# Optimization experiments

Measured on AMD Instinct MI355X. Metric: run time of the kernel, lower is better.

## Reference

```python
import jax, jax.numpy as jnp
import numpy as np

B, S, D, H, WINDOW = 2, 2048, 2048, 16, 256
HD = D // H  # head_dim = 128

def setup_inputs() -> dict:
    key = jax.random.key(0)
    ks = jax.random.split(key, 6)
    s = 0.02  # initializer_range-like scale for weights
    return {
        "hidden_states": jax.random.normal(ks[0], (B, S, D), jnp.float32),
        "attention_mask": jnp.ones((B, S), jnp.int32),
        "Wq": jax.random.normal(ks[1], (D, D), jnp.float32) * s,
        "Wk": jax.random.normal(ks[2], (D, D), jnp.float32) * s,
        "Wv": jax.random.normal(ks[3], (D, D), jnp.float32) * s,
        "Wo": jax.random.normal(ks[4], (D, D), jnp.float32) * s,
        "bo": jnp.zeros((D,), jnp.float32),
    }

def reference(hidden_states, attention_mask, Wq, Wk, Wv, Wo, bo):
    # GPT-Neo quirk: query is multiplied by sqrt(head_dim) and then
    # dot_product_attention_weights divides by sqrt(head_dim) -> net UNSCALED scores.
    q = (hidden_states @ Wq).reshape(B, S, H, HD)  # [B,S,H,hd]
    k = (hidden_states @ Wk).reshape(B, S, H, HD)
    v = (hidden_states @ Wv).reshape(B, S, H, HD)

    # local causal mask: attend iff i - window < j <= i
    i = jnp.arange(S)[:, None]
    j = jnp.arange(S)[None, :]
    local_causal = (j <= i) & (j > i - WINDOW)  # [S,S]
    mask = local_causal[None, None] & (attention_mask[:, None, None, :] > 0)  # [B,1,S,S]

    neg = jnp.finfo(jnp.float32).min
    scores = jnp.einsum("bqhd,bkhd->bhqk", q, k)  # [B,H,S,S] unscaled
    scores = jnp.where(mask, scores, neg)
    attn = jax.nn.softmax(scores, axis=-1)

    out = jnp.einsum("bhqk,bkhd->bqhd", attn, v).reshape(B, S, D)
    return out @ Wo + bo
```

## Files before the change

### kernel.cpp

```cpp
#include <hip/hip_runtime.h>

#define B_   2
#define S_   2048
#define D_   2048
#define H_   16
#define HD_  128
#define WIN_ 256
#define M_   (B_ * S_)

typedef float  f32x4  __attribute__((ext_vector_type(4)));
typedef short  s16x8  __attribute__((ext_vector_type(8)));
typedef __bf16 bf16x8 __attribute__((ext_vector_type(8)));
typedef unsigned short ushort_t;

__device__ inline unsigned short f2b(float f) {
  unsigned u = __builtin_bit_cast(unsigned, f);
  u += 0x7fffu + ((u >> 16) & 1u);
  return (unsigned short)(u >> 16);
}
__device__ inline float b2f(unsigned short h) {
  unsigned u = ((unsigned)h) << 16;
  return __builtin_bit_cast(float, u);
}

template <typename T>
__device__ auto mfma_impl(T a, T b, f32x4 c, int)
    -> decltype(__builtin_amdgcn_mfma_f32_16x16x32_bf16(a, b, c, 0, 0, 0)) {
  return __builtin_amdgcn_mfma_f32_16x16x32_bf16(a, b, c, 0, 0, 0);
}
template <typename T>
__device__ f32x4 mfma_impl(T a, T b, f32x4 c, long) {
  return __builtin_amdgcn_mfma_f32_16x16x32_bf16(
      __builtin_bit_cast(bf16x8, a), __builtin_bit_cast(bf16x8, b), c, 0, 0, 0);
}
__device__ inline f32x4 mfma_bf16(s16x8 a, s16x8 b, f32x4 c) {
  return mfma_impl(a, b, c, 0);
}

#if defined(__has_builtin)
#if __has_builtin(__builtin_amdgcn_global_load_lds)
#define HAS_GLL 1
#endif
#endif
#ifndef HAS_GLL
#define HAS_GLL 0
#endif

__device__ inline void gl_lds16(const ushort_t* g, ushort_t* lds_wave_base) {
#if HAS_GLL
  __builtin_amdgcn_global_load_lds(
      (const __attribute__((address_space(1))) unsigned int*)g,
      (__attribute__((address_space(3))) unsigned int*)lds_wave_base, 16, 0, 0);
#else
  const int lane = threadIdx.x & 63;
  *(uint4*)(lds_wave_base + lane * 8) = *(const uint4*)g;
#endif
}

__global__ __launch_bounds__(256) void k_split(const float* __restrict__ x,
                                               ushort_t* __restrict__ hi,
                                               ushort_t* __restrict__ lo, int n) {
  int i = (blockIdx.x * 256 + threadIdx.x) * 4;
  if (i + 3 < n) {
    float4 v = *(const float4*)(x + i);
    ushort4 h, l;
    h.x = f2b(v.x); l.x = f2b(v.x - b2f(h.x));
    h.y = f2b(v.y); l.y = f2b(v.y - b2f(h.y));
    h.z = f2b(v.z); l.z = f2b(v.z - b2f(h.z));
    h.w = f2b(v.w); l.w = f2b(v.w - b2f(h.w));
    *(ushort4*)(hi + i) = h;
    *(ushort4*)(lo + i) = l;
  }
}

__global__ __launch_bounds__(256) void k_transpose4(const float* __restrict__ W0,
                                                    const float* __restrict__ W1,
                                                    const float* __restrict__ W2,
                                                    const float* __restrict__ W3,
                                                    ushort_t* __restrict__ T0h,
                                                    ushort_t* __restrict__ T0l,
                                                    ushort_t* __restrict__ T1h,
                                                    ushort_t* __restrict__ T1l,
                                                    ushort_t* __restrict__ T2h,
                                                    ushort_t* __restrict__ T3h) {
  __shared__ float t[32][33];
  const int z = blockIdx.z;
  const float* W = (z == 0) ? W0 : (z == 1) ? W1 : (z == 2) ? W2 : W3;
  ushort_t* Th = (z == 0) ? T0h : (z == 1) ? T1h : (z == 2) ? T2h : T3h;
  ushort_t* Tl = (z == 0) ? T0l : (z == 1) ? T1l : nullptr;
  int bx = blockIdx.x * 32, by = blockIdx.y * 32;
  int tx = threadIdx.x, ty = threadIdx.y;
#pragma unroll
  for (int r = 0; r < 32; r += 8)
    t[ty + r][tx] = W[(size_t)(by + ty + r) * D_ + bx + tx];
  __syncthreads();
#pragma unroll
  for (int r = 0; r < 32; r += 8) {
    float v = t[tx][ty + r];
    unsigned short h = f2b(v);
    Th[(size_t)(bx + ty + r) * D_ + by + tx] = h;
    if (Tl) Tl[(size_t)(bx + ty + r) * D_ + by + tx] = f2b(v - b2f(h));
  }
}

__global__ __launch_bounds__(256) void k_vtrans(const ushort_t* __restrict__ Vb,
                                                ushort_t* __restrict__ Vt) {
  __shared__ ushort_t t[32][33];
  int bx = blockIdx.x * 32, by = blockIdx.y * 32, b = blockIdx.z;
  int tx = threadIdx.x, ty = threadIdx.y;
#pragma unroll
  for (int r = 0; r < 32; r += 8)
    t[ty + r][tx] = Vb[((size_t)(b * S_ + by + ty + r)) * D_ + bx + tx];
  __syncthreads();
#pragma unroll
  for (int r = 0; r < 32; r += 8)
    Vt[((size_t)(b * D_ + bx + ty + r)) * S_ + by + tx] = t[tx][ty + r];
}


__device__ inline void stage64(const ushort_t* __restrict__ g, int rowbase,
                               ushort_t* ldsTile, int tid) {
  const int r = tid >> 3;
  const int gs = ((tid & 7) ^ (r & 7)) * 8;
  gl_lds16(g + (size_t)(rowbase + r) * D_ + gs,
           ldsTile + rowbase * 64 + (tid >> 6) * 512);
}

__global__ __launch_bounds__(512) void k_qkv(
    const ushort_t* __restrict__ Ah, const ushort_t* __restrict__ Al,
    const ushort_t* __restrict__ WqH, const ushort_t* __restrict__ WqL,
    const ushort_t* __restrict__ WkH, const ushort_t* __restrict__ WvH,
    ushort_t* __restrict__ Qh, ushort_t* __restrict__ Ql,
    ushort_t* __restrict__ Ko, ushort_t* __restrict__ Vo) {
  __shared__ ushort_t Ab_[2][256 * 64];
  __shared__ ushort_t Bb_[2][256 * 64];
  const int tid = threadIdx.x;
  const int wave = tid >> 6, lane = tid & 63;
  const int quad = lane >> 4, l16 = lane & 15;

  const int lid = blockIdx.y * 24 + blockIdx.x;
  const int nlid = (lid & 7) * 48 + (lid >> 3);
  const int bx = nlid % 24, by = nlid / 24;
  const int m0 = by * 256;
  const int wtype = bx >> 3;
  const int n0 = (bx & 7) * 256;
  const int nseg = (wtype == 0) ? 3 : (wtype == 1) ? 2 : 1;
  const ushort_t* Bh0 = (wtype == 0) ? WqH : (wtype == 1) ? WkH : WvH;
  const int NT = nseg << 5;
  const int NI = NT >> 1;

  const int wrM = (wave >> 2) * 128;
  const int wcN = (wave & 3) * 64;
  const int ko0 = (quad ^ (l16 & 7)) * 8;
  const int ko1 = ((4 + quad) ^ (l16 & 7)) * 8;

#define SRC_A(t) ((((t) >> 5) == 1 ? Al : Ah) + (size_t)m0 * D_ + ((t) & 31) * 64)
#define SRC_B(t) ((((t) >> 5) == 2 ? WqL : Bh0) + (size_t)n0 * D_ + ((t) & 31) * 64)
#define RD(buf, row, ko) (*(const s16x8*)((buf) + (row) * 64 + (ko)))

  {
    const ushort_t* sA0 = SRC_A(0);
    const ushort_t* sB0 = SRC_B(0);
    const ushort_t* sB1 = SRC_B(1);
    stage64(sA0, 0,   &Ab_[0][0], tid); stage64(sA0, 64,  &Ab_[0][0], tid);
    stage64(sA0, 128, &Ab_[0][0], tid); stage64(sA0, 192, &Ab_[0][0], tid);
    stage64(sB0, 0,   &Bb_[0][0], tid); stage64(sB0, 64,  &Bb_[0][0], tid);
    stage64(sB0, 128, &Bb_[0][0], tid); stage64(sB0, 192, &Bb_[0][0], tid);
    stage64(sB1, 0,   &Bb_[1][0], tid); stage64(sB1, 64,  &Bb_[1][0], tid);
    stage64(sB1, 128, &Bb_[1][0], tid); stage64(sB1, 192, &Bb_[1][0], tid);
  }
  asm volatile("s_waitcnt vmcnt(4)" ::: "memory");
  __builtin_amdgcn_s_barrier();
  asm volatile("" ::: "memory");

#define PH_PRE()                                         \
  __builtin_amdgcn_s_barrier();                          \
  asm volatile("s_waitcnt lgkmcnt(0)" ::: "memory");     \
  __builtin_amdgcn_sched_barrier(0);                     \
  __builtin_amdgcn_s_setprio(1)
#define PH_POST()                                        \
  __builtin_amdgcn_s_setprio(0);                         \
  __builtin_amdgcn_s_barrier();                          \
  asm volatile("" ::: "memory")

  f32x4 acc[8][4] = {};
  s16x8 aF[4][2], bL[2][2], bH[2][2];

  for (int i = 0; i < NI; ++i) {
    const int t0 = 2 * i;
    const bool doSt = (i + 1 < NI);
    const ushort_t* A0 = &Ab_[0][0];
    const ushort_t* B0 = &Bb_[0][0];
    const ushort_t* A1 = &Ab_[1][0];
    const ushort_t* B1 = &Bb_[1][0];
    const ushort_t* sAt1 = SRC_A(t0 + 1);
    const ushort_t* sAt2 = SRC_A(t0 + 2);
    const ushort_t* sBt2 = SRC_B(t0 + 2);
    const ushort_t* sBt3 = SRC_B(t0 + 3);

#pragma unroll
    for (int f = 0; f < 4; ++f) {
      aF[f][0] = RD(A0, wrM + f * 16 + l16, ko0);
      aF[f][1] = RD(A0, wrM + f * 16 + l16, ko1);
    }
#pragma unroll
    for (int c = 0; c < 2; ++c) {
      bL[c][0] = RD(B0, wcN + c * 16 + l16, ko0);
      bL[c][1] = RD(B0, wcN + c * 16 + l16, ko1);
    }
    stage64(sAt1, 0, &Ab_[1][0], tid);
    stage64(sAt1, 64, &Ab_[1][0], tid);
    PH_PRE();
#pragma unroll
    for (int f = 0; f < 4; ++f)
#pragma unroll
      for (int c = 0; c < 2; ++c) {
        acc[f][c] = mfma_bf16(aF[f][0], bL[c][0], acc[f][c]);
        acc[f][c] = mfma_bf16(aF[f][1], bL[c][1], acc[f][c]);
      }
    PH_POST();

#pragma unroll
    for (int c = 0; c < 2; ++c) {
      bH[c][0] = RD(B0, wcN + 32 + c * 16 + l16, ko0);
      bH[c][1] = RD(B0, wcN + 32 + c * 16 + l16, ko1);
    }
    stage64(sAt1, 128, &Ab_[1][0], tid);
    stage64(sAt1, 192, &Ab_[1][0], tid);
    PH_PRE();
#pragma unroll
    for (int f = 0; f < 4; ++f)
#pragma unroll
      for (int c = 0; c < 2; ++c) {
        acc[f][2 + c] = mfma_bf16(aF[f][0], bH[c][0], acc[f][2 + c]);
        acc[f][2 + c] = mfma_bf16(aF[f][1], bH[c][1], acc[f][2 + c]);
      }
    PH_POST();

#pragma unroll
    for (int f = 0; f < 4; ++f) {
      aF[f][0] = RD(A0, wrM + 64 + f * 16 + l16, ko0);
      aF[f][1] = RD(A0, wrM + 64 + f * 16 + l16, ko1);
    }
    if (doSt) {
      stage64(sBt2, 0, &Bb_[0][0], tid);
      stage64(sBt2, 64, &Bb_[0][0], tid);
    }
    PH_PRE();
#pragma unroll
    for (int f = 0; f < 4; ++f)
#pragma unroll
      for (int c = 0; c < 2; ++c) {
        acc[4 + f][c] = mfma_bf16(aF[f][0], bL[c][0], acc[4 + f][c]);
        acc[4 + f][c] = mfma_bf16(aF[f][1], bL[c][1], acc[4 + f][c]);
      }
    PH_POST();

    if (doSt) {
      stage64(sBt2, 128, &Bb_[0][0], tid);
      stage64(sBt2, 192, &Bb_[0][0], tid);
    }
    PH_PRE();
#pragma unroll
    for (int f = 0; f < 4; ++f)
#pragma unroll
      for (int c = 0; c < 2; ++c) {
        acc[4 + f][2 + c] = mfma_bf16(aF[f][0], bH[c][0], acc[4 + f][2 + c]);
        acc[4 + f][2 + c] = mfma_bf16(aF[f][1], bH[c][1], acc[4 + f][2 + c]);
      }
    __builtin_amdgcn_s_setprio(0);
    if (doSt) asm volatile("s_waitcnt vmcnt(4)" ::: "memory");
    else      asm volatile("s_waitcnt vmcnt(0)" ::: "memory");
    __builtin_amdgcn_s_barrier();
    asm volatile("" ::: "memory");

#pragma unroll
    for (int f = 0; f < 4; ++f) {
      aF[f][0] = RD(A1, wrM + f * 16 + l16, ko0);
      aF[f][1] = RD(A1, wrM + f * 16 + l16, ko1);
    }
#pragma unroll
    for (int c = 0; c < 2; ++c) {
      bL[c][0] = RD(B1, wcN + c * 16 + l16, ko0);
      bL[c][1] = RD(B1, wcN + c * 16 + l16, ko1);
    }
    if (doSt) {
      stage64(sAt2, 0, &Ab_[0][0], tid);
      stage64(sAt2, 64, &Ab_[0][0], tid);
    }
    PH_PRE();
#pragma unroll
    for (int f = 0; f < 4; ++f)
#pragma unroll
      for (int c = 0; c < 2; ++c) {
        acc[f][c] = mfma_bf16(aF[f][0], bL[c][0], acc[f][c]);
        acc[f][c] = mfma_bf16(aF[f][1], bL[c][1], acc[f][c]);
      }
    PH_POST();

#pragma unroll
    for (int c = 0; c < 2; ++c) {
      bH[c][0] = RD(B1, wcN + 32 + c * 16 + l16, ko0);
      bH[c][1] = RD(B1, wcN + 32 + c * 16 + l16, ko1);
    }
    if (doSt) {
      stage64(sAt2, 128, &Ab_[0][0], tid);
      stage64(sAt2, 192, &Ab_[0][0], tid);
    }
    PH_PRE();
#pragma unroll
    for (int f = 0; f < 4; ++f)
#pragma unroll
      for (int c = 0; c < 2; ++c) {
        acc[f][2 + c] = mfma_bf16(aF[f][0], bH[c][0], acc[f][2 + c]);
        acc[f][2 + c] = mfma_bf16(aF[f][1], bH[c][1], acc[f][2 + c]);
      }
    PH_POST();

#pragma unroll
    for (int f = 0; f < 4; ++f) {
      aF[f][0] = RD(A1, wrM + 64 + f * 16 + l16, ko0);
      aF[f][1] = RD(A1, wrM + 64 + f * 16 + l16, ko1);
    }
    if (doSt) {
      stage64(sBt3, 0, &Bb_[1][0], tid);
      stage64(sBt3, 64, &Bb_[1][0], tid);
    }
    PH_PRE();
#pragma unroll
    for (int f = 0; f < 4; ++f)
#pragma unroll
      for (int c = 0; c < 2; ++c) {
        acc[4 + f][c] = mfma_bf16(aF[f][0], bL[c][0], acc[4 + f][c]);
        acc[4 + f][c] = mfma_bf16(aF[f][1], bL[c][1], acc[4 + f][c]);
      }
    PH_POST();

    if (doSt) {
      stage64(sBt3, 128, &Bb_[1][0], tid);
      stage64(sBt3, 192, &Bb_[1][0], tid);
    }
    PH_PRE();
#pragma unroll
    for (int f = 0; f < 4; ++f)
#pragma unroll
      for (int c = 0; c < 2; ++c) {
        acc[4 + f][2 + c] = mfma_bf16(aF[f][0], bH[c][0], acc[4 + f][2 + c]);
        acc[4 + f][2 + c] = mfma_bf16(aF[f][1], bH[c][1], acc[4 + f][2 + c]);
      }
    __builtin_amdgcn_s_setprio(0);
    if (doSt) {
      asm volatile("s_waitcnt vmcnt(4)" ::: "memory");
      __builtin_amdgcn_s_barrier();
      asm volatile("" ::: "memory");
    }
  }
#undef PH_PRE
#undef PH_POST
#undef SRC_A
#undef SRC_B
#undef RD

#pragma unroll
  for (int a = 0; a < 8; ++a)
#pragma unroll
    for (int nt = 0; nt < 4; ++nt)
#pragma unroll
      for (int r = 0; r < 4; ++r) {
        const int row = m0 + wrM + a * 16 + quad * 4 + r;
        const int col = n0 + wcN + nt * 16 + l16;
        const float v = acc[a][nt][r];
        const size_t idx = (size_t)row * D_ + col;
        if (wtype == 0) {
          unsigned short h = f2b(v);
          Qh[idx] = h;
          Ql[idx] = f2b(v - b2f(h));
        } else if (wtype == 1) {
          Ko[idx] = f2b(v);
        } else {
          Vo[idx] = f2b(v);
        }
      }
}

__device__ inline void stage_chunk(const ushort_t* __restrict__ gbase, int K,
                                   int rowbase, ushort_t* ldsTile, int tid) {
  const int rr = tid >> 3;
  const int gs = ((tid & 7) ^ (rr & 7)) * 8;
  gl_lds16(gbase + (size_t)(rowbase + rr) * K + gs,
           ldsTile + rowbase * 64 + (tid >> 6) * 512);
}

template <int NSEG, int OUT>
__global__ __launch_bounds__(512) void k_gemm8(
    const ushort_t* __restrict__ A0, const ushort_t* __restrict__ A1,
    const ushort_t* __restrict__ A2, const ushort_t* __restrict__ B0,
    const ushort_t* __restrict__ B2, ushort_t* __restrict__ Co,
    ushort_t* __restrict__ Col, float* __restrict__ Cf,
    const float* __restrict__ bias, int M, int N, int K) {
  __shared__ ushort_t As_[3][256 * 64];
  __shared__ ushort_t Bs_[3][128 * 64];
  const int tid = threadIdx.x;
  const int wave = tid >> 6, lane = tid & 63;
  const int quad = lane >> 4, l16 = lane & 15;
  const int m0 = blockIdx.y * 256, n0 = blockIdx.x * 128;
  const int wrM = (wave >> 1) * 64;
  const int wcN = (wave & 1) * 64;
  const int aRowB = (wrM + l16) * 64;
  const int bRowB = (wcN + l16) * 64;
  int ks8[2];
  ks8[0] = ((0 + quad) ^ (l16 & 7)) * 8;
  ks8[1] = ((4 + quad) ^ (l16 & 7)) * 8;
  const int NT = NSEG * 32;

  {
    const ushort_t* Ab0 = A0 + (size_t)m0 * K;
    const ushort_t* Bb0 = B0 + (size_t)n0 * K;
#pragma unroll
    for (int t = 0; t < 2; ++t) {
      const ushort_t* Ab = Ab0 + t * 64;
      const ushort_t* Bb = Bb0 + t * 64;
      stage_chunk(Ab, K, 0,   &As_[t][0], tid);
      stage_chunk(Ab, K, 64,  &As_[t][0], tid);
      stage_chunk(Ab, K, 128, &As_[t][0], tid);
      stage_chunk(Ab, K, 192, &As_[t][0], tid);
      stage_chunk(Bb, K, 0,   &Bs_[t][0], tid);
      stage_chunk(Bb, K, 64,  &Bs_[t][0], tid);
    }
  }
  asm volatile("s_waitcnt vmcnt(6)" ::: "memory");
  __builtin_amdgcn_s_barrier();
  asm volatile("" ::: "memory");

  f32x4 acc[4][4] = {};
  int cur = 0;
  for (int kt = 0; kt < NT; ++kt) {
    const int st = kt + 2;
    const bool doStage = (st < NT);
    int sbuf = cur + 2; if (sbuf >= 3) sbuf -= 3;
    ushort_t* At  = &As_[cur][0];
    ushort_t* Bt  = &Bs_[cur][0];
    ushort_t* Ads = &As_[sbuf][0];
    ushort_t* Bds = &Bs_[sbuf][0];
    const ushort_t* Asb = A0;
    const ushort_t* Bsb = B0;
    if (doStage) {
      const int sg = st >> 5;
      const ushort_t* Ag = A0;
      const ushort_t* Bg = B0;
      if (NSEG >= 2 && sg == 1) Ag = A1;
      if (NSEG == 3 && sg == 2) { Ag = A2; Bg = B2; }
      Asb = Ag + (size_t)m0 * K + (size_t)(st & 31) * 64;
      Bsb = Bg + (size_t)n0 * K + (size_t)(st & 31) * 64;
    }
    s16x8 bf[4][2];
#pragma unroll
    for (int p = 0; p < 2; ++p) {
      s16x8 af[2][2];
#pragma unroll
      for (int i = 0; i < 2; ++i)
#pragma unroll
        for (int s = 0; s < 2; ++s)
          af[i][s] = *(const s16x8*)(At + aRowB + (p * 2 + i) * 1024 + ks8[s]);
      if (p == 0) {
#pragma unroll
        for (int nt = 0; nt < 4; ++nt)
#pragma unroll
          for (int s = 0; s < 2; ++s)
            bf[nt][s] = *(const s16x8*)(Bt + bRowB + nt * 1024 + ks8[s]);
      }
      if (doStage) {
        if (p == 0) {
          stage_chunk(Asb, K, 0,   Ads, tid);
          stage_chunk(Asb, K, 64,  Ads, tid);
          stage_chunk(Asb, K, 128, Ads, tid);
        } else {
          stage_chunk(Asb, K, 192, Ads, tid);
          stage_chunk(Bsb, K, 0,   Bds, tid);
          stage_chunk(Bsb, K, 64,  Bds, tid);
        }
      }
      asm volatile("s_waitcnt lgkmcnt(0)" ::: "memory");
      __builtin_amdgcn_sched_barrier(0);
      __builtin_amdgcn_s_setprio(1);
#pragma unroll
      for (int i = 0; i < 2; ++i)
#pragma unroll
        for (int nt = 0; nt < 4; ++nt)
#pragma unroll
          for (int s = 0; s < 2; ++s)
            acc[p * 2 + i][nt] = mfma_bf16(af[i][s], bf[nt][s], acc[p * 2 + i][nt]);
      __builtin_amdgcn_s_setprio(0);
      if (p == 1) {
        if (doStage) asm volatile("s_waitcnt vmcnt(6)" ::: "memory");
        else         asm volatile("s_waitcnt vmcnt(0)" ::: "memory");
        __builtin_amdgcn_s_barrier();
        asm volatile("" ::: "memory");
      }
    }
    cur = (cur == 2) ? 0 : cur + 1;
  }

#pragma unroll
  for (int mt = 0; mt < 4; ++mt)
#pragma unroll
    for (int nt = 0; nt < 4; ++nt)
#pragma unroll
      for (int r = 0; r < 4; ++r) {
        int row = m0 + wrM + mt * 16 + quad * 4 + r;
        int col = n0 + wcN + nt * 16 + l16;
        float v = acc[mt][nt][r];
        if (OUT == 2) {
          Cf[(size_t)row * N + col] = v + bias[col];
        } else if (OUT == 1) {
          unsigned short h = f2b(v);
          Co[(size_t)row * N + col]  = h;
          Col[(size_t)row * N + col] = f2b(v - b2f(h));
        } else {
          Co[(size_t)row * N + col] = f2b(v);
        }
      }
}

__global__ __launch_bounds__(256) void k_fattn(const ushort_t* __restrict__ Qh,
                                               const ushort_t* __restrict__ Ql,
                                               const ushort_t* __restrict__ Kh,
                                               const ushort_t* __restrict__ Vt,
                                               const int* __restrict__ amask,
                                               ushort_t* __restrict__ AO) {
  __shared__ ushort_t Ksh[64][136];
  __shared__ ushort_t Vs[128][72];
  __shared__ ushort_t ps[4][16][72];
  __shared__ int ams[320];
  const int tid = threadIdx.x;
  const int wave = tid >> 6, lane = tid & 63;
  const int quad = lane >> 4, l16 = lane & 15;
  const int qt = blockIdx.x, h = blockIdx.y, b = blockIdx.z;
  const int q0 = qt * 64;

  for (int x = tid; x < 320; x += 256) {
    int j = q0 - 256 + x;
    ams[x] = (j >= 0) ? amask[b * S_ + j] : 0;
  }

  const int qrowA = q0 + wave * 16 + l16;
  const ushort_t* qbh = Qh + ((size_t)(b * S_ + qrowA) * D_) + h * HD_;
  const ushort_t* qbl = Ql + ((size_t)(b * S_ + qrowA) * D_) + h * HD_;
  s16x8 qh[4], ql[4];
#pragma unroll
  for (int kk = 0; kk < 4; kk++) {
    qh[kk] = *(const s16x8*)(qbh + kk * 32 + quad * 8);
    ql[kk] = *(const s16x8*)(qbl + kk * 32 + quad * 8);
  }

  f32x4 O[8] = {};
  float m_run[4], l_run[4];
#pragma unroll
  for (int r = 0; r < 4; r++) { m_run[r] = -3.0e38f; l_run[r] = 0.f; }

  const int t0 = (qt < 4) ? (4 - qt) : 0;
  for (int t = t0; t < 5; t++) {
    const int kb = q0 - 256 + 64 * t;
    __syncthreads();
    {
      const int key = tid >> 2, dimb = (tid & 3) * 32;
      const ushort_t* kgh = Kh + ((size_t)(b * S_ + kb + key) * D_) + h * HD_ + dimb;
#pragma unroll
      for (int u = 0; u < 4; u++)
        *(uint4*)&Ksh[key][dimb + u * 8] = *(const uint4*)(kgh + u * 8);
      const int hd = tid >> 1, keyb = (tid & 1) * 32;
      const ushort_t* vg = Vt + ((size_t)(b * D_ + h * HD_ + hd) * S_) + kb + keyb;
#pragma unroll
      for (int u = 0; u < 4; u++)
        *(uint4*)&Vs[hd][keyb + u * 8] = *(const uint4*)(vg + u * 8);
    }
    __syncthreads();

    f32x4 sacc[4] = {};
#pragma unroll
    for (int kk = 0; kk < 4; kk++)
#pragma unroll
      for (int nt = 0; nt < 4; nt++) {
        s16x8 kfh = *(const s16x8*)&Ksh[nt * 16 + l16][kk * 32 + quad * 8];
        sacc[nt] = mfma_bf16(qh[kk], kfh, sacc[nt]);
        sacc[nt] = mfma_bf16(ql[kk], kfh, sacc[nt]);
      }

#pragma unroll
    for (int nt = 0; nt < 4; nt++) {
      const int j = kb + nt * 16 + l16;
      const bool amok = ams[64 * t + nt * 16 + l16] != 0;
#pragma unroll
      for (int r = 0; r < 4; r++) {
        const int iq = q0 + wave * 16 + quad * 4 + r;
        const bool ok = amok && (j <= iq) && (j > iq - WIN_);
        if (!ok) sacc[nt][r] = -3.0e38f;
      }
    }
    float mt[4];
#pragma unroll
    for (int r = 0; r < 4; r++) {
      mt[r] = fmaxf(fmaxf(sacc[0][r], sacc[1][r]), fmaxf(sacc[2][r], sacc[3][r]));
      mt[r] = fmaxf(mt[r], __shfl_xor(mt[r], 1));
      mt[r] = fmaxf(mt[r], __shfl_xor(mt[r], 2));
      mt[r] = fmaxf(mt[r], __shfl_xor(mt[r], 4));
      mt[r] = fmaxf(mt[r], __shfl_xor(mt[r], 8));
    }
    float alpha[4], lt[4];
#pragma unroll
    for (int r = 0; r < 4; r++) {
      float mnew = fmaxf(m_run[r], mt[r]);
      alpha[r] = __expf(m_run[r] - mnew);
      m_run[r] = mnew;
      lt[r] = 0.f;
#pragma unroll
      for (int nt = 0; nt < 4; nt++) {
        float s = sacc[nt][r];
        float p = (s > -1.0e30f) ? __expf(s - mnew) : 0.f;
        sacc[nt][r] = p;
        lt[r] += p;
      }
      lt[r] += __shfl_xor(lt[r], 1);
      lt[r] += __shfl_xor(lt[r], 2);
      lt[r] += __shfl_xor(lt[r], 4);
      lt[r] += __shfl_xor(lt[r], 8);
      l_run[r] = l_run[r] * alpha[r] + lt[r];
    }
#pragma unroll
    for (int o = 0; o < 8; o++)
#pragma unroll
      for (int r = 0; r < 4; r++) O[o][r] *= alpha[r];
#pragma unroll
    for (int nt = 0; nt < 4; nt++)
#pragma unroll
      for (int r = 0; r < 4; r++)
        ps[wave][quad * 4 + r][nt * 16 + l16] = f2b(sacc[nt][r]);
    __syncthreads();
#pragma unroll
    for (int kk2 = 0; kk2 < 2; kk2++) {
      s16x8 pf = *(const s16x8*)&ps[wave][l16][kk2 * 32 + quad * 8];
#pragma unroll
      for (int o = 0; o < 8; o++) {
        s16x8 vf = *(const s16x8*)&Vs[o * 16 + l16][kk2 * 32 + quad * 8];
        O[o] = mfma_bf16(pf, vf, O[o]);
      }
    }
  }
#pragma unroll
  for (int r = 0; r < 4; r++) l_run[r] = 1.0f / l_run[r];
#pragma unroll
  for (int o = 0; o < 8; o++)
#pragma unroll
    for (int r = 0; r < 4; r++) {
      int row = q0 + wave * 16 + quad * 4 + r;
      AO[((size_t)(b * S_ + row) * D_) + h * HD_ + o * 16 + l16] = f2b(O[o][r] * l_run[r]);
    }
}

extern "C" void kernel_launch(void* const* d_in, const int* in_sizes, int n_in,
                              void* d_out, int out_size, void* d_ws, size_t ws_size,
                              hipStream_t stream) {
  const float* hs    = (const float*)d_in[0];
  const int*   amask = (const int*)d_in[1];
  const float* Wq    = (const float*)d_in[2];
  const float* Wk    = (const float*)d_in[3];
  const float* Wv    = (const float*)d_in[4];
  const float* Wo    = (const float*)d_in[5];
  const float* bo    = (const float*)d_in[6];
  float* out = (float*)d_out;

  char* p = (char*)d_ws;
  ushort_t* hsHi = (ushort_t*)p; p += (size_t)16 << 20;
  ushort_t* hsLo = (ushort_t*)p; p += (size_t)16 << 20;
  ushort_t* WqTh = (ushort_t*)p; p += (size_t)8 << 20;
  ushort_t* WqTl = (ushort_t*)p; p += (size_t)8 << 20;
  ushort_t* WkTh = (ushort_t*)p; p += (size_t)8 << 20;
  ushort_t* WkTl = (ushort_t*)p; p += (size_t)8 << 20;  (void)WkTl;
  ushort_t* WvTh = (ushort_t*)p; p += (size_t)8 << 20;
  ushort_t* WoTh = (ushort_t*)p; p += (size_t)8 << 20;
  ushort_t* Qhb  = (ushort_t*)p; p += (size_t)16 << 20;
  ushort_t* Qlb  = (ushort_t*)p; p += (size_t)16 << 20;
  ushort_t* Khb  = (ushort_t*)p; p += (size_t)16 << 20;
  ushort_t* Vb   = (ushort_t*)p; p += (size_t)16 << 20;
  ushort_t* Vt   = (ushort_t*)p; p += (size_t)16 << 20;

  k_split<<<M_ * D_ / 1024, 256, 0, stream>>>(hs, hsHi, hsLo, M_ * D_);
  dim3 tb(32, 8), tg4(D_ / 32, D_ / 32, 4);
  k_transpose4<<<tg4, tb, 0, stream>>>(Wq, Wk, Wv, Wo, WqTh, WqTl, WkTh, nullptr, WvTh, WoTh);

  dim3 gq(24, 16);
  k_qkv<<<gq, 512, 0, stream>>>(hsHi, hsLo, WqTh, WqTl, WkTh, WvTh, Qhb, Qlb, Khb, Vb);

  dim3 vg(D_ / 32, S_ / 32, B_);
  k_vtrans<<<vg, tb, 0, stream>>>(Vb, Vt);

  dim3 ag(S_ / 64, H_, B_);
  k_fattn<<<ag, 256, 0, stream>>>(Qhb, Qlb, Khb, Vt, amask, hsHi );

  dim3 gg(D_ / 128, M_ / 256);
  k_gemm8<1, 2><<<gg, 512, 0, stream>>>(hsHi , nullptr, nullptr, WoTh, nullptr,
                                        nullptr, nullptr, out, bo, M_, D_, D_);
}
```

Measured before the change: 426.7 us.

## Double-buffer K/V tiles with register prefetch in sliding-window attention kernel

The attention kernel now handles 128 query rows per block with 512 threads instead of 64 rows with 256. K and V tiles sit in two LDS buffers, and the next tile is prefetched into registers while the current one is computed; the tile loop is unrolled in pairs and uses s_setprio around the MFMA sections. The goal is to hide global-load latency behind compute and to reuse each staged K/V tile across more query rows. In exchange it uses more LDS and registers per block and launches fewer blocks, which may reduce occupancy.

```diff
diff --git a/kernel.cpp b/kernel.cpp
--- a/kernel.cpp
+++ b/kernel.cpp
@@ -116,7 +116,6 @@
   for (int r = 0; r < 32; r += 8)
     Vt[((size_t)(b * D_ + bx + ty + r)) * S_ + by + tx] = t[tx][ty + r];
 }
-
 
 __device__ inline void stage64(const ushort_t* __restrict__ g, int rowbase,
                                ushort_t* ldsTile, int tid) {
@@ -522,26 +521,32 @@
       }
 }
 
-__global__ __launch_bounds__(256) void k_fattn(const ushort_t* __restrict__ Qh,
+__global__ __launch_bounds__(512) void k_fattn(const ushort_t* __restrict__ Qh,
                                                const ushort_t* __restrict__ Ql,
                                                const ushort_t* __restrict__ Kh,
                                                const ushort_t* __restrict__ Vt,
                                                const int* __restrict__ amask,
                                                ushort_t* __restrict__ AO) {
-  __shared__ ushort_t Ksh[64][136];
-  __shared__ ushort_t Vs[128][72];
-  __shared__ ushort_t ps[4][16][72];
-  __shared__ int ams[320];
+  __shared__ ushort_t Ksh[2][64][136];
+  __shared__ ushort_t Vs[2][128][72];
+  __shared__ ushort_t ps[8][16][72];
+  __shared__ int ams[384];
   const int tid = threadIdx.x;
   const int wave = tid >> 6, lane = tid & 63;
   const int quad = lane >> 4, l16 = lane & 15;
   const int qt = blockIdx.x, h = blockIdx.y, b = blockIdx.z;
-  const int q0 = qt * 64;
-
-  for (int x = tid; x < 320; x += 256) {
+  const int q0 = qt * 128;
+  const int t0 = (qt < 2) ? (4 - 2 * qt) : 0;
+
+  for (int x = tid; x < 384; x += 512) {
     int j = q0 - 256 + x;
     ams[x] = (j >= 0) ? amask[b * S_ + j] : 0;
   }
+
+  const int key  = tid >> 3, dimb = (tid & 7) * 16;
+  const int hd   = tid >> 2, keyb = (tid & 3) * 16;
+  const ushort_t* kgT = Kh + ((size_t)(b * S_) + key) * D_ + h * HD_ + dimb;
+  const ushort_t* vgT = Vt + ((size_t)(b * D_ + h * HD_ + hd)) * S_ + keyb;
 
   const int qrowA = q0 + wave * 16 + l16;
   const ushort_t* qbh = Qh + ((size_t)(b * S_ + qrowA) * D_) + h * HD_;
@@ -558,94 +563,120 @@
 #pragma unroll
   for (int r = 0; r < 4; r++) { m_run[r] = -3.0e38f; l_run[r] = 0.f; }
 
-  const int t0 = (qt < 4) ? (4 - qt) : 0;
-  for (int t = t0; t < 5; t++) {
-    const int kb = q0 - 256 + 64 * t;
-    __syncthreads();
-    {
-      const int key = tid >> 2, dimb = (tid & 3) * 32;
-      const ushort_t* kgh = Kh + ((size_t)(b * S_ + kb + key) * D_) + h * HD_ + dimb;
-#pragma unroll
-      for (int u = 0; u < 4; u++)
-        *(uint4*)&Ksh[key][dimb + u * 8] = *(const uint4*)(kgh + u * 8);
-      const int hd = tid >> 1, keyb = (tid & 1) * 32;
-      const ushort_t* vg = Vt + ((size_t)(b * D_ + h * HD_ + hd) * S_) + kb + keyb;
-#pragma unroll
-      for (int u = 0; u < 4; u++)
-        *(uint4*)&Vs[hd][keyb + u * 8] = *(const uint4*)(vg + u * 8);
-    }
-    __syncthreads();
-
-    f32x4 sacc[4] = {};
-#pragma unroll
-    for (int kk = 0; kk < 4; kk++)
-#pragma unroll
-      for (int nt = 0; nt < 4; nt++) {
-        s16x8 kfh = *(const s16x8*)&Ksh[nt * 16 + l16][kk * 32 + quad * 8];
-        sacc[nt] = mfma_bf16(qh[kk], kfh, sacc[nt]);
-        sacc[nt] = mfma_bf16(ql[kk], kfh, sacc[nt]);
-      }
-
-#pragma unroll
-    for (int nt = 0; nt < 4; nt++) {
-      const int j = kb + nt * 16 + l16;
-      const bool amok = ams[64 * t + nt * 16 + l16] != 0;
-#pragma unroll
-      for (int r = 0; r < 4; r++) {
-        const int iq = q0 + wave * 16 + quad * 4 + r;
-        const bool ok = amok && (j <= iq) && (j > iq - WIN_);
-        if (!ok) sacc[nt][r] = -3.0e38f;
-      }
-    }
-    float mt[4];
-#pragma unroll
-    for (int r = 0; r < 4; r++) {
-      mt[r] = fmaxf(fmaxf(sacc[0][r], sacc[1][r]), fmaxf(sacc[2][r], sacc[3][r]));
-      mt[r] = fmaxf(mt[r], __shfl_xor(mt[r], 1));
-      mt[r] = fmaxf(mt[r], __shfl_xor(mt[r], 2));
-      mt[r] = fmaxf(mt[r], __shfl_xor(mt[r], 4));
-      mt[r] = fmaxf(mt[r], __shfl_xor(mt[r], 8));
-    }
-    float alpha[4], lt[4];
-#pragma unroll
-    for (int r = 0; r < 4; r++) {
-      float mnew = fmaxf(m_run[r], mt[r]);
-      alpha[r] = __expf(m_run[r] - mnew);
-      m_run[r] = mnew;
-      lt[r] = 0.f;
-#pragma unroll
-      for (int nt = 0; nt < 4; nt++) {
-        float s = sacc[nt][r];
-        float p = (s > -1.0e30f) ? __expf(s - mnew) : 0.f;
-        sacc[nt][r] = p;
-        lt[r] += p;
-      }
-      lt[r] += __shfl_xor(lt[r], 1);
-      lt[r] += __shfl_xor(lt[r], 2);
-      lt[r] += __shfl_xor(lt[r], 4);
-      lt[r] += __shfl_xor(lt[r], 8);
-      l_run[r] = l_run[r] * alpha[r] + lt[r];
-    }
-#pragma unroll
-    for (int o = 0; o < 8; o++)
-#pragma unroll
-      for (int r = 0; r < 4; r++) O[o][r] *= alpha[r];
-#pragma unroll
-    for (int nt = 0; nt < 4; nt++)
-#pragma unroll
-      for (int r = 0; r < 4; r++)
-        ps[wave][quad * 4 + r][nt * 16 + l16] = f2b(sacc[nt][r]);
-    __syncthreads();
-#pragma unroll
-    for (int kk2 = 0; kk2 < 2; kk2++) {
-      s16x8 pf = *(const s16x8*)&ps[wave][l16][kk2 * 32 + quad * 8];
-#pragma unroll
-      for (int o = 0; o < 8; o++) {
-        s16x8 vf = *(const s16x8*)&Vs[o * 16 + l16][kk2 * 32 + quad * 8];
-        O[o] = mfma_bf16(pf, vf, O[o]);
-      }
-    }
-  }
+  uint4 rAk0, rAk1, rAv0, rAv1, rBk0, rBk1, rBv0, rBv1;
+  {
+    const long kb0 = (long)q0 - 256 + 64 * t0;
+    const ushort_t* kg = kgT + kb0 * D_;
+    const ushort_t* vg = vgT + kb0;
+    uint4 k0 = *(const uint4*)kg, k1 = *(const uint4*)(kg + 8);
+    uint4 v0 = *(const uint4*)vg, v1 = *(const uint4*)(vg + 8);
+    *(uint4*)&Ksh[0][key][dimb]     = k0;
+    *(uint4*)&Ksh[0][key][dimb + 8] = k1;
+    *(uint4*)&Vs[0][hd][keyb]       = v0;
+    *(uint4*)&Vs[0][hd][keyb + 8]   = v1;
+    const long kb1 = kb0 + 64;
+    const ushort_t* kg1 = kgT + kb1 * D_;
+    const ushort_t* vg1 = vgT + kb1;
+    rBk0 = *(const uint4*)kg1; rBk1 = *(const uint4*)(kg1 + 8);
+    rBv0 = *(const uint4*)vg1; rBv1 = *(const uint4*)(vg1 + 8);
+  }
+  asm volatile("s_waitcnt lgkmcnt(0)" ::: "memory");
+  __builtin_amdgcn_s_barrier();
+  asm volatile("" ::: "memory");
+
+#define FA_TILE(T, P, Wk0, Wk1, Wv0, Wv1, Ik0, Ik1, Iv0, Iv1)                   \
+  do {                                                                          \
+    if ((T) + 1 <= 5) {                                                         \
+      *(uint4*)&Ksh[(P) ^ 1][key][dimb]     = Wk0;                              \
+      *(uint4*)&Ksh[(P) ^ 1][key][dimb + 8] = Wk1;                              \
+      *(uint4*)&Vs[(P) ^ 1][hd][keyb]       = Wv0;                              \
+      *(uint4*)&Vs[(P) ^ 1][hd][keyb + 8]   = Wv1;                              \
+    }                                                                           \
+    if ((T) + 2 <= 5) {                                                         \
+      const long kb2 = (long)q0 - 256 + 64 * ((T) + 2);                         \
+      const ushort_t* kg2 = kgT + kb2 * D_;                                     \
+      const ushort_t* vg2 = vgT + kb2;                                          \
+      Ik0 = *(const uint4*)kg2; Ik1 = *(const uint4*)(kg2 + 8);                 \
+      Iv0 = *(const uint4*)vg2; Iv1 = *(const uint4*)(vg2 + 8);                 \
+    }                                                                           \
+    asm volatile("s_waitcnt lgkmcnt(0)" ::: "memory");                          \
+    __builtin_amdgcn_s_barrier();                                               \
+    asm volatile("" ::: "memory");                                              \
+    {                                                                           \
+      const int kb = q0 - 256 + 64 * (T);                                       \
+      f32x4 sacc[4] = {};                                                       \
+      __builtin_amdgcn_s_setprio(1);                                            \
+      _Pragma("unroll") for (int kk = 0; kk < 4; kk++)                          \
+        _Pragma("unroll") for (int nt = 0; nt < 4; nt++) {                      \
+          s16x8 kfh = *(const s16x8*)&Ksh[P][nt * 16 + l16][kk * 32 + quad * 8];\
+          sacc[nt] = mfma_bf16(qh[kk], kfh, sacc[nt]);                          \
+          sacc[nt] = mfma_bf16(ql[kk], kfh, sacc[nt]);                          \
+        }                                                                       \
+      __builtin_amdgcn_s_setprio(0);                                            \
+      _Pragma("unroll") for (int nt = 0; nt < 4; nt++) {                        \
+        const int j = kb + nt * 16 + l16;                                       \
+        const bool amok = ams[64 * (T) + nt * 16 + l16] != 0;                   \
+        _Pragma("unroll") for (int r = 0; r < 4; r++) {                         \
+          const int iq = q0 + wave * 16 + quad * 4 + r;                         \
+          const bool ok = amok && (j <= iq) && (j > iq - WIN_);                 \
+          if (!ok) sacc[nt][r] = -3.0e38f;                                      \
+        }                                                                       \
+      }                                                                         \
+      float mt[4];                                                              \
+      _Pragma("unroll") for (int r = 0; r < 4; r++) {                           \
+        mt[r] = fmaxf(fmaxf(sacc[0][r], sacc[1][r]),                            \
+                      fmaxf(sacc[2][r], sacc[3][r]));                           \
+        mt[r] = fmaxf(mt[r], __shfl_xor(mt[r], 1));                             \
+        mt[r] = fmaxf(mt[r], __shfl_xor(mt[r], 2));                             \
+        mt[r] = fmaxf(mt[r], __shfl_xor(mt[r], 4));                             \
+        mt[r] = fmaxf(mt[r], __shfl_xor(mt[r], 8));                             \
+      }                                                                         \
+      float alpha[4], lt[4];                                                    \
+      _Pragma("unroll") for (int r = 0; r < 4; r++) {                           \
+        float mnew = fmaxf(m_run[r], mt[r]);                                    \
+        alpha[r] = __expf(m_run[r] - mnew);                                     \
+        m_run[r] = mnew;                                                        \
+        lt[r] = 0.f;                                                            \
+        _Pragma("unroll") for (int nt = 0; nt < 4; nt++) {                      \
+          float s = sacc[nt][r];                                                \
+          float p = (s > -1.0e30f) ? __expf(s - mnew) : 0.f;                    \
+          sacc[nt][r] = p;                                                      \
+          lt[r] += p;                                                           \
+        }                                                                       \
+        lt[r] += __shfl_xor(lt[r], 1);                                          \
+        lt[r] += __shfl_xor(lt[r], 2);                                          \
+        lt[r] += __shfl_xor(lt[r], 4);                                          \
+        lt[r] += __shfl_xor(lt[r], 8);                                          \
+        l_run[r] = l_run[r] * alpha[r] + lt[r];                                 \
+      }                                                                         \
+      _Pragma("unroll") for (int o = 0; o < 8; o++)                             \
+        _Pragma("unroll") for (int r = 0; r < 4; r++) O[o][r] *= alpha[r];      \
+      _Pragma("unroll") for (int nt = 0; nt < 4; nt++)                          \
+        _Pragma("unroll") for (int r = 0; r < 4; r++)                           \
+          ps[wave][quad * 4 + r][nt * 16 + l16] = f2b(sacc[nt][r]);             \
+      asm volatile("s_waitcnt lgkmcnt(0)" ::: "memory");                        \
+      __builtin_amdgcn_s_barrier();                                             \
+      asm volatile("" ::: "memory");                                            \
+      __builtin_amdgcn_s_setprio(1);                                            \
+      _Pragma("unroll") for (int kk2 = 0; kk2 < 2; kk2++) {                     \
+        s16x8 pf = *(const s16x8*)&ps[wave][l16][kk2 * 32 + quad * 8];          \
+        _Pragma("unroll") for (int o = 0; o < 8; o++) {                         \
+          s16x8 vf = *(const s16x8*)&Vs[P][o * 16 + l16][kk2 * 32 + quad * 8];  \
+          O[o] = mfma_bf16(pf, vf, O[o]);                                       \
+        }                                                                       \
+      }                                                                         \
+      __builtin_amdgcn_s_setprio(0);                                            \
+      __builtin_amdgcn_s_barrier();                                             \
+      asm volatile("" ::: "memory");                                            \
+    }                                                                           \
+  } while (0)
+
+  for (int t = t0; t <= 5; t += 2) {
+    FA_TILE(t,     0, rBk0, rBk1, rBv0, rBv1, rAk0, rAk1, rAv0, rAv1);
+    FA_TILE(t + 1, 1, rAk0, rAk1, rAv0, rAv1, rBk0, rBk1, rBv0, rBv1);
+  }
+#undef FA_TILE
+
 #pragma unroll
   for (int r = 0; r < 4; r++) l_run[r] = 1.0f / l_run[r];
 #pragma unroll
@@ -694,8 +725,8 @@
   dim3 vg(D_ / 32, S_ / 32, B_);
   k_vtrans<<<vg, tb, 0, stream>>>(Vb, Vt);
 
-  dim3 ag(S_ / 64, H_, B_);
-  k_fattn<<<ag, 256, 0, stream>>>(Qhb, Qlb, Khb, Vt, amask, hsHi );
+  dim3 ag(S_ / 128, H_, B_);
+  k_fattn<<<ag, 512, 0, stream>>>(Qhb, Qlb, Khb, Vt, amask, hsHi );
 
   dim3 gg(D_ / 128, M_ / 256);
   k_gemm8<1, 2><<<gg, 512, 0, stream>>>(hsHi , nullptr, nullptr, WoTh, nullptr,
```

Measured after the change: 435.0 us. No clear change (+2.0%).
